# Kernel tuning notes

Measured on AMD Instinct MI355X. Metric: run time of the kernel, lower is better.

## Reference

```python
import jax, jax.numpy as jnp
import numpy as np

NUM_SAMPLE = 10


def setup_inputs() -> dict:
    key = jax.random.key(0)
    k1, k2, k3, k4, k5 = jax.random.split(key, 5)
    N, F, B, S = 100000, 256, 20000, NUM_SAMPLE
    features_ue = jax.random.normal(k1, (N, F), dtype=jnp.float32)
    features_ap = jax.random.normal(k2, (N, F), dtype=jnp.float32)
    neigh_idx = jax.random.randint(k3, (B, S), 0, N, dtype=jnp.int32)
    nodes = jax.random.randint(k4, (B,), 0, N, dtype=jnp.int32)
    # xavier-uniform weight [embed_dim, feature_dim] = [256, 2*F]
    embed_dim, feature_dim = 256, 2 * F
    limit = float(np.sqrt(6.0 / (embed_dim + feature_dim)))
    weight = jax.random.uniform(k5, (embed_dim, feature_dim), dtype=jnp.float32,
                                minval=-limit, maxval=limit)
    return {"features_ue": features_ue, "features_ap": features_ap,
            "neigh_idx": neigh_idx, "nodes": nodes, "weight": weight}


def reference(features_ue, features_ap, neigh_idx, nodes, weight):
    # sample_model='ue2ue': other_feature = self_feature = features_ue
    S = neigh_idx.shape[1]
    # gather sampled neighbor features: [B, S, F] -> sum over S
    gathered = jnp.take(features_ue, neigh_idx, axis=0)
    # original: mask.div(num_neigh + 1), i.e. divide by count PLUS one
    neigh_feats = gathered.sum(axis=1) / jnp.float32(S + 1)  # [B, F]
    self_feats = jnp.take(features_ue, nodes, axis=0)        # [B, F]
    combined = jnp.concatenate([self_feats, neigh_feats], axis=1)  # [B, 2F]
    # weight.mm(combined.t()) then relu -> [embed_dim, B]
    out = jax.nn.relu(jnp.einsum('ef,bf->eb', weight, combined))
    return out
```

## Files before the change

kernel.cpp:

```cpp
#include <hip/hip_runtime.h>

typedef __attribute__((ext_vector_type(8))) short short8;
typedef __attribute__((ext_vector_type(4))) float f32x4;

#define B_TOTAL 20000
#define BT      16
#define NBLK    1250
#define NF      256
#define K2      512
#define NS      10

__device__ __forceinline__ unsigned short f2bf(float x) {
    unsigned u = __builtin_bit_cast(unsigned, x);
    u += 0x7FFFu + ((u >> 16) & 1u);
    return (unsigned short)(u >> 16);
}

__global__ __launch_bounds__(256) void wconvert(const float* __restrict__ w,
                                                unsigned short* __restrict__ wbf) {
    const int i = (blockIdx.x * 256 + threadIdx.x) * 4;
    const float4 v = *(const float4*)(w + i);
    ushort4 o;
    o.x = f2bf(v.x); o.y = f2bf(v.y); o.z = f2bf(v.z); o.w = f2bf(v.w);
    *(ushort4*)(wbf + i) = o;
}

__global__ __launch_bounds__(256, 4) void fused(
    const float* __restrict__ ue, const int* __restrict__ nidx,
    const int* __restrict__ nodes, const unsigned short* __restrict__ wbf,
    float* __restrict__ out)
{
    __shared__ unsigned short comb[BT * K2];
    const int t    = threadIdx.x;
    const int lane = t & 63;
    const int wv   = t >> 6;
    const int bbase = blockIdx.x * BT;

    {
        const int r0 = wv * 4;
        const int b0 = bbase + r0;
        int nv = 0;
        if (lane < 40)      nv = nidx[b0 * NS + lane];
        else if (lane < 44) nv = nodes[b0 + (lane - 40)];

        for (int r = 0; r < 4; ++r) {
            const int row = r0 + r;
            const int nd  = __shfl(nv, 40 + r);
            const float4 sf = ((const float4*)(ue + (size_t)nd * NF))[lane];
            float ax = 0.f, ay = 0.f, az = 0.f, aw = 0.f;
            #pragma unroll
            for (int s = 0; s < NS; ++s) {
                const int is = __shfl(nv, r * NS + s);
                const float4 v = ((const float4*)(ue + (size_t)is * NF))[lane];
                ax += v.x; ay += v.y; az += v.z; aw += v.w;
            }
            const float inv = 1.0f / 11.0f;
            ushort4 s4, n4;
            s4.x = f2bf(sf.x); s4.y = f2bf(sf.y); s4.z = f2bf(sf.z); s4.w = f2bf(sf.w);
            n4.x = f2bf(ax * inv); n4.y = f2bf(ay * inv);
            n4.z = f2bf(az * inv); n4.w = f2bf(aw * inv);
            const int swz = (row & 7) << 4;
            char* base = (char*)comb + row * 1024;
            *(ushort4*)(base + ((lane * 8)       ^ swz)) = s4;
            *(ushort4*)(base + ((512 + lane * 8) ^ swz)) = n4;
        }
    }
    __syncthreads();

    const int fr = lane & 15;
    const int kq = lane >> 4;
    const unsigned short* wp = wbf + (size_t)(wv * 64 + fr) * K2 + kq * 8;
    const char* cbase = (const char*)comb + fr * 1024;
    const int swzR = (fr & 7) << 4;

    f32x4 acc[4] = {};
    #pragma unroll 4
    for (int ks = 0; ks < 16; ++ks) {
        const short8 bg = *(const short8*)(cbase + ((ks * 64 + kq * 16) ^ swzR));
        short8 af[4];
        #pragma unroll
        for (int i = 0; i < 4; ++i)
            af[i] = *(const short8*)(wp + (size_t)i * 16 * K2 + ks * 32);
        #pragma unroll
        for (int i = 0; i < 4; ++i)
            acc[i] = __builtin_amdgcn_mfma_f32_16x16x32_bf16(af[i], bg, acc[i], 0, 0, 0);
    }

    const int col = bbase + fr;
    #pragma unroll
    for (int i = 0; i < 4; ++i) {
        const int e = wv * 64 + i * 16 + kq * 4;
        #pragma unroll
        for (int r = 0; r < 4; ++r)
            out[(size_t)(e + r) * B_TOTAL + col] = fmaxf(acc[i][r], 0.0f);
    }
}

extern "C" void kernel_launch(void* const* d_in, const int* in_sizes, int n_in,
                              void* d_out, int out_size, void* d_ws, size_t ws_size,
                              hipStream_t stream) {
    const float* ue    = (const float*)d_in[0];
    const int*   nidx  = (const int*)d_in[2];
    const int*   nodes = (const int*)d_in[3];
    const float* w     = (const float*)d_in[4];
    float*       out   = (float*)d_out;

    unsigned short* wbf = (unsigned short*)d_ws;

    hipLaunchKernelGGL(wconvert, dim3(128), dim3(256), 0, stream, w, wbf);
    hipLaunchKernelGGL(fused, dim3(NBLK), dim3(256), 0, stream,
                       ue, nidx, nodes, wbf, out);
}
```

Baseline: 67.60 us.

## Pre-convert the whole feature table to bf16 before the gather

Adds a prep kernel that converts the entire 100000x256 fp32 feature table, plus the weight matrix, to bf16 in workspace on every call. The fused kernel then gathers half-width rows and accumulates the neighbour sum in fp32 from bf16 values. The aim is to halve the bytes moved by the random-row gather. The cost is a full-table read and write pass each call, and slightly lower precision because each neighbour is rounded before summing. If the workspace is too small, it falls back to the old path.

```diff
diff --git a/kernel.cpp b/kernel.cpp
--- a/kernel.cpp
+++ b/kernel.cpp
@@ -9,11 +9,39 @@
 #define NF      256
 #define K2      512
 #define NS      10
+#define N_NODES 100000
 
 __device__ __forceinline__ unsigned short f2bf(float x) {
     unsigned u = __builtin_bit_cast(unsigned, x);
     u += 0x7FFFu + ((u >> 16) & 1u);
     return (unsigned short)(u >> 16);
+}
+__device__ __forceinline__ float bf2f(unsigned short u) {
+    return __builtin_bit_cast(float, ((unsigned)u) << 16);
+}
+
+__global__ __launch_bounds__(256) void prep(
+    const float* __restrict__ ue, const float* __restrict__ w,
+    unsigned short* __restrict__ ueb, unsigned short* __restrict__ wbf)
+{
+    const int t = threadIdx.x, blk = blockIdx.x;
+    if (blk < 12500) {
+        const size_t i = ((size_t)blk * 256 + t) * 8;
+        const float4 v0 = *(const float4*)(ue + i);
+        const float4 v1 = *(const float4*)(ue + i + 4);
+        short8 o;
+        o[0] = (short)f2bf(v0.x); o[1] = (short)f2bf(v0.y);
+        o[2] = (short)f2bf(v0.z); o[3] = (short)f2bf(v0.w);
+        o[4] = (short)f2bf(v1.x); o[5] = (short)f2bf(v1.y);
+        o[6] = (short)f2bf(v1.z); o[7] = (short)f2bf(v1.w);
+        *(short8*)(ueb + i) = o;
+    } else {
+        const int base = (blk - 12500) * 1024 + t * 4;
+        const float4 v = *(const float4*)(w + base);
+        ushort4 o;
+        o.x = f2bf(v.x); o.y = f2bf(v.y); o.z = f2bf(v.z); o.w = f2bf(v.w);
+        *(ushort4*)(wbf + base) = o;
+    }
 }
 
 __global__ __launch_bounds__(256) void wconvert(const float* __restrict__ w,
@@ -25,8 +53,9 @@
     *(ushort4*)(wbf + i) = o;
 }
 
+template<int UEB>
 __global__ __launch_bounds__(256, 4) void fused(
-    const float* __restrict__ ue, const int* __restrict__ nidx,
+    const void* __restrict__ uev, const int* __restrict__ nidx,
     const int* __restrict__ nodes, const unsigned short* __restrict__ wbf,
     float* __restrict__ out)
 {
@@ -46,22 +75,37 @@
         for (int r = 0; r < 4; ++r) {
             const int row = r0 + r;
             const int nd  = __shfl(nv, 40 + r);
-            const float4 sf = ((const float4*)(ue + (size_t)nd * NF))[lane];
+            const int swz = (row & 7) << 4;
+            char* base = (char*)comb + row * 1024;
             float ax = 0.f, ay = 0.f, az = 0.f, aw = 0.f;
-            #pragma unroll
-            for (int s = 0; s < NS; ++s) {
-                const int is = __shfl(nv, r * NS + s);
-                const float4 v = ((const float4*)(ue + (size_t)is * NF))[lane];
-                ax += v.x; ay += v.y; az += v.z; aw += v.w;
+            if (UEB) {
+                const unsigned short* ueb = (const unsigned short*)uev;
+                const ushort4 sv = ((const ushort4*)(ueb + (size_t)nd * NF))[lane];
+                #pragma unroll
+                for (int s = 0; s < NS; ++s) {
+                    const int is = __shfl(nv, r * NS + s);
+                    const ushort4 a = ((const ushort4*)(ueb + (size_t)is * NF))[lane];
+                    ax += bf2f(a.x); ay += bf2f(a.y); az += bf2f(a.z); aw += bf2f(a.w);
+                }
+                *(ushort4*)(base + ((lane * 8) ^ swz)) = sv;
+            } else {
+                const float* ue = (const float*)uev;
+                const float4 sf = ((const float4*)(ue + (size_t)nd * NF))[lane];
+                #pragma unroll
+                for (int s = 0; s < NS; ++s) {
+                    const int is = __shfl(nv, r * NS + s);
+                    const float4 v = ((const float4*)(ue + (size_t)is * NF))[lane];
+                    ax += v.x; ay += v.y; az += v.z; aw += v.w;
+                }
+                ushort4 s4;
+                s4.x = f2bf(sf.x); s4.y = f2bf(sf.y);
+                s4.z = f2bf(sf.z); s4.w = f2bf(sf.w);
+                *(ushort4*)(base + ((lane * 8) ^ swz)) = s4;
             }
             const float inv = 1.0f / 11.0f;
-            ushort4 s4, n4;
-            s4.x = f2bf(sf.x); s4.y = f2bf(sf.y); s4.z = f2bf(sf.z); s4.w = f2bf(sf.w);
+            ushort4 n4;
             n4.x = f2bf(ax * inv); n4.y = f2bf(ay * inv);
             n4.z = f2bf(az * inv); n4.w = f2bf(aw * inv);
-            const int swz = (row & 7) << 4;
-            char* base = (char*)comb + row * 1024;
-            *(ushort4*)(base + ((lane * 8)       ^ swz)) = s4;
             *(ushort4*)(base + ((512 + lane * 8) ^ swz)) = n4;
         }
     }
@@ -105,9 +149,19 @@
     const float* w     = (const float*)d_in[4];
     float*       out   = (float*)d_out;
 
-    unsigned short* wbf = (unsigned short*)d_ws;
+    const size_t ueb_elems = (size_t)N_NODES * NF;
+    const size_t need = (ueb_elems + 256 * K2) * sizeof(unsigned short);
 
-    hipLaunchKernelGGL(wconvert, dim3(128), dim3(256), 0, stream, w, wbf);
-    hipLaunchKernelGGL(fused, dim3(NBLK), dim3(256), 0, stream,
-                       ue, nidx, nodes, wbf, out);
+    if (ws_size >= need) {
+        unsigned short* ueb = (unsigned short*)d_ws;
+        unsigned short* wbf = ueb + ueb_elems;
+        hipLaunchKernelGGL(prep, dim3(12628), dim3(256), 0, stream, ue, w, ueb, wbf);
+        hipLaunchKernelGGL((fused<1>), dim3(NBLK), dim3(256), 0, stream,
+                           (const void*)ueb, nidx, nodes, wbf, out);
+    } else {
+        unsigned short* wbf = (unsigned short*)d_ws;
+        hipLaunchKernelGGL(wconvert, dim3(128), dim3(256), 0, stream, w, wbf);
+        hipLaunchKernelGGL((fused<0>), dim3(NBLK), dim3(256), 0, stream,
+                           (const void*)ue, nidx, nodes, wbf, out);
+    }
 }
```

Result: slower. 76.46 us (+13.1%).
